# Performance work log

Hardware: AMD Instinct MI355X
Metric: run time of the kernel (lower is better)

Reference implementation:

```python
import jax, jax.numpy as jnp
import numpy as np

VOCAB, EMB, HID, OUT = 100000, 300, 512, 1
B, SEQ = 1, 512


def setup_inputs() -> dict:
    key = jax.random.key(0)
    ks = jax.random.split(key, 8)
    s = 1.0 / np.sqrt(HID)  # torch LSTMCell/Linear init scale
    return {
        "x": jax.random.randint(ks[0], (B, SEQ), 0, VOCAB),
        "h0": jnp.zeros((B, HID), jnp.float32),
        "c0": jnp.zeros((B, HID), jnp.float32),
        "emb_table": jax.random.normal(ks[1], (VOCAB, EMB), jnp.float32) * 0.1,
        "W_ih": jax.random.uniform(ks[2], (4 * HID, EMB), jnp.float32, -s, s),
        "W_hh": jax.random.uniform(ks[3], (4 * HID, HID), jnp.float32, -s, s),
        "b_ih": jax.random.uniform(ks[4], (4 * HID,), jnp.float32, -s, s),
        "b_hh": jax.random.uniform(ks[5], (4 * HID,), jnp.float32, -s, s),
        "fc_w": jax.random.uniform(ks[6], (OUT, HID), jnp.float32, -s, s),
        "fc_b": jax.random.uniform(ks[7], (OUT,), jnp.float32, -s, s),
    }


def reference(x, h0, c0, emb_table, W_ih, W_hh, b_ih, b_hh, fc_w, fc_b):
    embeds = emb_table[x]                      # [B, SEQ, EMB]
    # Faithful to torch: embeds[0][i].view(B, EMB) for i in range(EMB); B == 1.
    steps = embeds[0, :EMB].reshape(EMB, B, EMB)  # [EMB steps, B, EMB]

    def cell(carry, xt):
        h, c = carry
        gates = xt @ W_ih.T + b_ih + h @ W_hh.T + b_hh   # [B, 4*HID]
        i, f, g, o = jnp.split(gates, 4, axis=-1)        # torch gate order i,f,g,o
        i = jax.nn.sigmoid(i)
        f = jax.nn.sigmoid(f)
        g = jnp.tanh(g)
        o = jax.nn.sigmoid(o)
        c = f * c + i * g
        h = o * jnp.tanh(c)
        return (h, c), None

    (h, c), _ = jax.lax.scan(cell, (h0, c0), steps)
    # dropout is identity in eval mode
    out = jax.nn.sigmoid(h @ fc_w.T + fc_b)   # [B, OUT]
    out = out.reshape(B, -1)[:, -1]           # [B]
    return (out, h, c)
```

## Files before the change

### kernel.cpp

```cpp
#include <hip/hip_runtime.h>

#define EMBD 300
#define NSTEP 300
#define HID 512
#define G4 2048
#define NWG 32
#define TPB 256

#define TS2 15
#define NSG 20
#define NRG 8

#define SENTINEL 0xFFC00000u

#define XP_SZ   (NSTEP * G4)
#define HSEQ_OFF XP_SZ

__device__ __forceinline__ float fsig(float x) { return 1.0f / (1.0f + __expf(-x)); }
__device__ __forceinline__ float ftanh(float x) {
    x = fminf(15.0f, fmaxf(-15.0f, x));
    float t = __expf(2.0f * x);
    return (t - 1.0f) / (t + 1.0f);
}

__global__ __launch_bounds__(TPB) void xproj_init_kernel(
    const int* __restrict__ x, const float* __restrict__ h0,
    const float* __restrict__ emb, const float* __restrict__ W_ih,
    const float* __restrict__ b_ih, const float* __restrict__ b_hh,
    float* __restrict__ ws) {
    const int rowg = blockIdx.x;
    const int sg   = blockIdx.y;
    const int tid  = threadIdx.x;
    const int t0   = sg * TS2;
    const int r    = rowg * TPB + tid;

    float* hseq = ws + HSEQ_OFF;

    if (rowg == 0) {
        unsigned* hs = (unsigned*)(hseq + (size_t)(t0 + 1) * HID);
        for (int i = tid; i < TS2 * HID; i += TPB) hs[i] = SENTINEL;
        if (sg == 0) {
            for (int i = tid; i < HID; i += TPB) hseq[i] = h0[i];
        }
    }

    __shared__ float e_lds[TS2][EMBD];
    for (int tt = 0; tt < TS2; ++tt) {
        const float* er = emb + (long long)x[t0 + tt] * EMBD;
        for (int i = tid; i < EMBD; i += TPB) e_lds[tt][i] = er[i];
    }
    __syncthreads();

    float acc[TS2];
    const float bsum = b_ih[r] + b_hh[r];
    #pragma unroll
    for (int tt = 0; tt < TS2; ++tt) acc[tt] = bsum;

    const float* wrow = W_ih + (size_t)r * EMBD;
    for (int e = 0; e < EMBD; e += 4) {
        const float4 w4 = *(const float4*)(wrow + e);
        #pragma unroll
        for (int tt = 0; tt < TS2; ++tt) {
            acc[tt] = fmaf(w4.x, e_lds[tt][e],     acc[tt]);
            acc[tt] = fmaf(w4.y, e_lds[tt][e + 1], acc[tt]);
            acc[tt] = fmaf(w4.z, e_lds[tt][e + 2], acc[tt]);
            acc[tt] = fmaf(w4.w, e_lds[tt][e + 3], acc[tt]);
        }
    }
    #pragma unroll
    for (int tt = 0; tt < TS2; ++tt)
        ws[(size_t)(t0 + tt) * G4 + r] = acc[tt];
}

__global__ __launch_bounds__(TPB, 1) void lstm_scan_kernel(
    const float* __restrict__ c0, const float* __restrict__ W_hh,
    const float* __restrict__ fc_w, const float* __restrict__ fc_b,
    float* __restrict__ ws, float* __restrict__ out) {
    const int tid  = threadIdx.x;
    const int wg   = blockIdx.x;
    const int v    = tid >> 6;
    const int lane = tid & 63;
    const int g    = lane >> 4;
    const int li   = lane & 15;
    const int hidx = wg * 16 + v * 4 + g;

    float* hseq    = ws + HSEQ_OFF;
    const float* xp = ws;

    __shared__ __align__(16) float h_lds[576];

    float wreg[4][32];
    #pragma unroll
    for (int gate = 0; gate < 4; ++gate) {
        const float* wr = W_hh + ((size_t)gate * HID + hidx) * HID + li * 32;
        #pragma unroll
        for (int k = 0; k < 32; k += 4) {
            const float4 w4 = *(const float4*)(wr + k);
            wreg[gate][k] = w4.x; wreg[gate][k + 1] = w4.y;
            wreg[gate][k + 2] = w4.z; wreg[gate][k + 3] = w4.w;
        }
    }

    const bool upd = (li == 0);
    float c = upd ? c0[hidx] : 0.0f;

    for (int s = 0; s < NSTEP; ++s) {
        float xi = 0.f, xf = 0.f, xg = 0.f, xo = 0.f;
        if (upd) {
            const float* xpt = xp + (size_t)s * G4 + hidx;
            xi = xpt[0]; xf = xpt[HID]; xg = xpt[2 * HID]; xo = xpt[3 * HID];
        }

        unsigned* hb = (unsigned*)(hseq + (size_t)s * HID);
        unsigned a = __hip_atomic_load(hb + tid,       __ATOMIC_RELAXED, __HIP_MEMORY_SCOPE_AGENT);
        unsigned b = __hip_atomic_load(hb + tid + 256, __ATOMIC_RELAXED, __HIP_MEMORY_SCOPE_AGENT);
        while (a == SENTINEL || b == SENTINEL) {
            __builtin_amdgcn_s_sleep(1);
            a = __hip_atomic_load(hb + tid,       __ATOMIC_RELAXED, __HIP_MEMORY_SCOPE_AGENT);
            b = __hip_atomic_load(hb + tid + 256, __ATOMIC_RELAXED, __HIP_MEMORY_SCOPE_AGENT);
        }
        const int i0 = tid, i1 = tid + 256;
        h_lds[i0 + ((i0 >> 5) << 2)] = __uint_as_float(a);
        h_lds[i1 + ((i1 >> 5) << 2)] = __uint_as_float(b);
        __syncthreads();

        float sums[4];
        const float* hrow = &h_lds[li * 36];
        #pragma unroll
        for (int gate = 0; gate < 4; ++gate) {
            float acc = 0.0f;
            #pragma unroll
            for (int k = 0; k < 32; k += 4) {
                const float4 h4 = *(const float4*)(hrow + k);
                acc = fmaf(wreg[gate][k],     h4.x, acc);
                acc = fmaf(wreg[gate][k + 1], h4.y, acc);
                acc = fmaf(wreg[gate][k + 2], h4.z, acc);
                acc = fmaf(wreg[gate][k + 3], h4.w, acc);
            }
            acc += __shfl_xor(acc, 1);
            acc += __shfl_xor(acc, 2);
            acc += __shfl_xor(acc, 4);
            acc += __shfl_xor(acc, 8);
            sums[gate] = acc;
        }

        if (upd) {
            const float iv = fsig(sums[0] + xi);
            const float fv = fsig(sums[1] + xf);
            const float gv = ftanh(sums[2] + xg);
            const float ov = fsig(sums[3] + xo);
            c = fv * c + iv * gv;
            const float h = ov * ftanh(c);
            __hip_atomic_store((unsigned*)(hseq + (size_t)(s + 1) * HID + hidx),
                               __float_as_uint(h),
                               __ATOMIC_RELAXED, __HIP_MEMORY_SCOPE_AGENT);
            if (s == NSTEP - 1) {
                out[1 + hidx] = h;
                out[1 + HID + hidx] = c;
            }
        }
        __syncthreads();
    }

    if (wg == 0) {
        __syncthreads();
        unsigned* hf = (unsigned*)(hseq + (size_t)NSTEP * HID);
        unsigned a = __hip_atomic_load(hf + tid,       __ATOMIC_RELAXED, __HIP_MEMORY_SCOPE_AGENT);
        unsigned b = __hip_atomic_load(hf + tid + 256, __ATOMIC_RELAXED, __HIP_MEMORY_SCOPE_AGENT);
        while (a == SENTINEL || b == SENTINEL) {
            __builtin_amdgcn_s_sleep(1);
            a = __hip_atomic_load(hf + tid,       __ATOMIC_RELAXED, __HIP_MEMORY_SCOPE_AGENT);
            b = __hip_atomic_load(hf + tid + 256, __ATOMIC_RELAXED, __HIP_MEMORY_SCOPE_AGENT);
        }
        float p = __uint_as_float(a) * fc_w[tid] + __uint_as_float(b) * fc_w[tid + 256];
        h_lds[tid] = p;
        __syncthreads();
        for (int off = 128; off > 0; off >>= 1) {
            if (tid < off) h_lds[tid] += h_lds[tid + off];
            __syncthreads();
        }
        if (tid == 0) out[0] = fsig(h_lds[0] + fc_b[0]);
    }
}

extern "C" void kernel_launch(void* const* d_in, const int* in_sizes, int n_in,
                              void* d_out, int out_size, void* d_ws, size_t ws_size,
                              hipStream_t stream) {
    (void)in_sizes; (void)n_in; (void)out_size; (void)ws_size;
    const int*   x     = (const int*)d_in[0];
    const float* h0    = (const float*)d_in[1];
    const float* c0    = (const float*)d_in[2];
    const float* emb   = (const float*)d_in[3];
    const float* W_ih  = (const float*)d_in[4];
    const float* W_hh  = (const float*)d_in[5];
    const float* b_ih  = (const float*)d_in[6];
    const float* b_hh  = (const float*)d_in[7];
    const float* fc_w  = (const float*)d_in[8];
    const float* fc_b  = (const float*)d_in[9];
    float* out = (float*)d_out;
    float* ws  = (float*)d_ws;

    xproj_init_kernel<<<dim3(NRG, NSG), dim3(TPB), 0, stream>>>(
        x, h0, emb, W_ih, b_ih, b_hh, ws);
    lstm_scan_kernel<<<dim3(NWG), dim3(TPB), 0, stream>>>(
        c0, W_hh, fc_w, fc_b, ws, out);
}
```

Before: 687.1 us.

## Split LSTM recurrence across 512 threads with double-buffered LDS and packed h exchange

```diff
diff --git a/kernel.cpp b/kernel.cpp
--- a/kernel.cpp
+++ b/kernel.cpp
@@ -4,8 +4,9 @@
 #define NSTEP 300
 #define HID 512
 #define G4 2048
+#define TPB1 256
+#define TPB2 512
 #define NWG 32
-#define TPB 256
 
 #define TS2 15
 #define NSG 20
@@ -13,7 +14,7 @@
 
 #define SENTINEL 0xFFC00000u
 
-#define XP_SZ   (NSTEP * G4)
+#define XP_SZ    (NSTEP * G4)
 #define HSEQ_OFF XP_SZ
 
 __device__ __forceinline__ float fsig(float x) { return 1.0f / (1.0f + __expf(-x)); }
@@ -23,7 +24,7 @@
     return (t - 1.0f) / (t + 1.0f);
 }
 
-__global__ __launch_bounds__(TPB) void xproj_init_kernel(
+__global__ __launch_bounds__(TPB1) void xproj_init_kernel(
     const int* __restrict__ x, const float* __restrict__ h0,
     const float* __restrict__ emb, const float* __restrict__ W_ih,
     const float* __restrict__ b_ih, const float* __restrict__ b_hh,
@@ -32,22 +33,22 @@
     const int sg   = blockIdx.y;
     const int tid  = threadIdx.x;
     const int t0   = sg * TS2;
-    const int r    = rowg * TPB + tid;
+    const int r    = rowg * TPB1 + tid;
 
     float* hseq = ws + HSEQ_OFF;
 
     if (rowg == 0) {
         unsigned* hs = (unsigned*)(hseq + (size_t)(t0 + 1) * HID);
-        for (int i = tid; i < TS2 * HID; i += TPB) hs[i] = SENTINEL;
+        for (int i = tid; i < TS2 * HID; i += TPB1) hs[i] = SENTINEL;
         if (sg == 0) {
-            for (int i = tid; i < HID; i += TPB) hseq[i] = h0[i];
+            for (int i = tid; i < HID; i += TPB1) hseq[i] = h0[i];
         }
     }
 
     __shared__ float e_lds[TS2][EMBD];
     for (int tt = 0; tt < TS2; ++tt) {
         const float* er = emb + (long long)x[t0 + tt] * EMBD;
-        for (int i = tid; i < EMBD; i += TPB) e_lds[tt][i] = er[i];
+        for (int i = tid; i < EMBD; i += TPB1) e_lds[tt][i] = er[i];
     }
     __syncthreads();
 
@@ -72,36 +73,36 @@
         ws[(size_t)(t0 + tt) * G4 + r] = acc[tt];
 }
 
-__global__ __launch_bounds__(TPB, 1) void lstm_scan_kernel(
+__global__ __launch_bounds__(TPB2, 1) void lstm_scan_kernel(
     const float* __restrict__ c0, const float* __restrict__ W_hh,
     const float* __restrict__ fc_w, const float* __restrict__ fc_b,
     float* __restrict__ ws, float* __restrict__ out) {
     const int tid  = threadIdx.x;
     const int wg   = blockIdx.x;
-    const int v    = tid >> 6;
     const int lane = tid & 63;
-    const int g    = lane >> 4;
-    const int li   = lane & 15;
-    const int hidx = wg * 16 + v * 4 + g;
-
-    float* hseq    = ws + HSEQ_OFF;
+    const int grp  = tid >> 5;
+    const int sub  = tid & 31;
+    const int gate = sub >> 3;
+    const int cl   = sub & 7;
+    const int hidx = wg * 16 + grp;
+
+    float* hseq     = ws + HSEQ_OFF;
     const float* xp = ws;
 
-    __shared__ __align__(16) float h_lds[576];
-
-    float wreg[4][32];
-    #pragma unroll
-    for (int gate = 0; gate < 4; ++gate) {
-        const float* wr = W_hh + ((size_t)gate * HID + hidx) * HID + li * 32;
+    __shared__ __align__(16) float h_lds[2][544];
+
+    float wreg[64];
+    {
+        const float* wr = W_hh + ((size_t)gate * HID + hidx) * HID + cl * 64;
         #pragma unroll
-        for (int k = 0; k < 32; k += 4) {
+        for (int k = 0; k < 64; k += 4) {
             const float4 w4 = *(const float4*)(wr + k);
-            wreg[gate][k] = w4.x; wreg[gate][k + 1] = w4.y;
-            wreg[gate][k + 2] = w4.z; wreg[gate][k + 3] = w4.w;
-        }
-    }
-
-    const bool upd = (li == 0);
+            wreg[k] = w4.x; wreg[k + 1] = w4.y;
+            wreg[k + 2] = w4.z; wreg[k + 3] = w4.w;
+        }
+    }
+
+    const bool upd = (sub == 0);
     float c = upd ? c0[hidx] : 0.0f;
 
     for (int s = 0; s < NSTEP; ++s) {
@@ -111,75 +112,89 @@
             xi = xpt[0]; xf = xpt[HID]; xg = xpt[2 * HID]; xo = xpt[3 * HID];
         }
 
-        unsigned* hb = (unsigned*)(hseq + (size_t)s * HID);
-        unsigned a = __hip_atomic_load(hb + tid,       __ATOMIC_RELAXED, __HIP_MEMORY_SCOPE_AGENT);
-        unsigned b = __hip_atomic_load(hb + tid + 256, __ATOMIC_RELAXED, __HIP_MEMORY_SCOPE_AGENT);
-        while (a == SENTINEL || b == SENTINEL) {
-            __builtin_amdgcn_s_sleep(1);
-            a = __hip_atomic_load(hb + tid,       __ATOMIC_RELAXED, __HIP_MEMORY_SCOPE_AGENT);
-            b = __hip_atomic_load(hb + tid + 256, __ATOMIC_RELAXED, __HIP_MEMORY_SCOPE_AGENT);
-        }
-        const int i0 = tid, i1 = tid + 256;
-        h_lds[i0 + ((i0 >> 5) << 2)] = __uint_as_float(a);
-        h_lds[i1 + ((i1 >> 5) << 2)] = __uint_as_float(b);
+        if (tid < 256) {
+            const unsigned long long* slot =
+                (const unsigned long long*)(hseq + (size_t)s * HID) + tid;
+            unsigned long long hv = __hip_atomic_load(slot, __ATOMIC_RELAXED,
+                                                      __HIP_MEMORY_SCOPE_AGENT);
+            while ((unsigned)hv == SENTINEL || (unsigned)(hv >> 32) == SENTINEL) {
+                __builtin_amdgcn_s_sleep(1);
+                hv = __hip_atomic_load(slot, __ATOMIC_RELAXED,
+                                       __HIP_MEMORY_SCOPE_AGENT);
+            }
+            const int i0 = 2 * tid + ((tid >> 5) << 2);
+            *(float2*)&h_lds[s & 1][i0] =
+                make_float2(__uint_as_float((unsigned)hv),
+                            __uint_as_float((unsigned)(hv >> 32)));
+        }
         __syncthreads();
 
-        float sums[4];
-        const float* hrow = &h_lds[li * 36];
+        float acc = 0.0f;
+        const float* hrow = &h_lds[s & 1][cl * 68];
         #pragma unroll
-        for (int gate = 0; gate < 4; ++gate) {
-            float acc = 0.0f;
-            #pragma unroll
-            for (int k = 0; k < 32; k += 4) {
-                const float4 h4 = *(const float4*)(hrow + k);
-                acc = fmaf(wreg[gate][k],     h4.x, acc);
-                acc = fmaf(wreg[gate][k + 1], h4.y, acc);
-                acc = fmaf(wreg[gate][k + 2], h4.z, acc);
-                acc = fmaf(wreg[gate][k + 3], h4.w, acc);
+        for (int k = 0; k < 64; k += 4) {
+            const float4 h4 = *(const float4*)(hrow + k);
+            acc = fmaf(wreg[k],     h4.x, acc);
+            acc = fmaf(wreg[k + 1], h4.y, acc);
+            acc = fmaf(wreg[k + 2], h4.z, acc);
+            acc = fmaf(wreg[k + 3], h4.w, acc);
+        }
+        acc += __shfl_xor(acc, 1);
+        acc += __shfl_xor(acc, 2);
+        acc += __shfl_xor(acc, 4);
+
+        const int base = lane & ~31;
+        const float gi = __shfl(acc, base + 0);
+        const float gf = __shfl(acc, base + 8);
+        const float gg = __shfl(acc, base + 16);
+        const float go = __shfl(acc, base + 24);
+
+        float hnew = 0.0f;
+        if (upd) {
+            const float iv = fsig(gi + xi);
+            const float fv = fsig(gf + xf);
+            const float gv = ftanh(gg + xg);
+            const float ov = fsig(go + xo);
+            c = fv * c + iv * gv;
+            hnew = ov * ftanh(c);
+        }
+        const float hhi = __shfl(hnew, (lane + 32) & 63);
+        if (lane == 0) {
+            const unsigned long long pair =
+                (unsigned long long)__float_as_uint(hnew) |
+                ((unsigned long long)__float_as_uint(hhi) << 32);
+            unsigned long long* dst =
+                (unsigned long long*)(hseq + (size_t)(s + 1) * HID + hidx);
+            __hip_atomic_store(dst, pair, __ATOMIC_RELAXED,
+                               __HIP_MEMORY_SCOPE_AGENT);
+        }
+        if (upd && s == NSTEP - 1) {
+            out[1 + hidx] = hnew;
+            out[1 + HID + hidx] = c;
+        }
+    }
+
+    if (wg == 0) {
+        __shared__ float red[256];
+        if (tid < 256) {
+            const unsigned long long* slot =
+                (const unsigned long long*)(hseq + (size_t)NSTEP * HID) + tid;
+            unsigned long long hv = __hip_atomic_load(slot, __ATOMIC_RELAXED,
+                                                      __HIP_MEMORY_SCOPE_AGENT);
+            while ((unsigned)hv == SENTINEL || (unsigned)(hv >> 32) == SENTINEL) {
+                __builtin_amdgcn_s_sleep(1);
+                hv = __hip_atomic_load(slot, __ATOMIC_RELAXED,
+                                       __HIP_MEMORY_SCOPE_AGENT);
             }
-            acc += __shfl_xor(acc, 1);
-            acc += __shfl_xor(acc, 2);
-            acc += __shfl_xor(acc, 4);
-            acc += __shfl_xor(acc, 8);
-            sums[gate] = acc;
-        }
-
-        if (upd) {
-            const float iv = fsig(sums[0] + xi);
-            const float fv = fsig(sums[1] + xf);
-            const float gv = ftanh(sums[2] + xg);
-            const float ov = fsig(sums[3] + xo);
-            c = fv * c + iv * gv;
-            const float h = ov * ftanh(c);
-            __hip_atomic_store((unsigned*)(hseq + (size_t)(s + 1) * HID + hidx),
-                               __float_as_uint(h),
-                               __ATOMIC_RELAXED, __HIP_MEMORY_SCOPE_AGENT);
-            if (s == NSTEP - 1) {
-                out[1 + hidx] = h;
-                out[1 + HID + hidx] = c;
-            }
-        }
-        __syncthreads();
-    }
-
-    if (wg == 0) {
-        __syncthreads();
-        unsigned* hf = (unsigned*)(hseq + (size_t)NSTEP * HID);
-        unsigned a = __hip_atomic_load(hf + tid,       __ATOMIC_RELAXED, __HIP_MEMORY_SCOPE_AGENT);
-        unsigned b = __hip_atomic_load(hf + tid + 256, __ATOMIC_RELAXED, __HIP_MEMORY_SCOPE_AGENT);
-        while (a == SENTINEL || b == SENTINEL) {
-            __builtin_amdgcn_s_sleep(1);
-            a = __hip_atomic_load(hf + tid,       __ATOMIC_RELAXED, __HIP_MEMORY_SCOPE_AGENT);
-            b = __hip_atomic_load(hf + tid + 256, __ATOMIC_RELAXED, __HIP_MEMORY_SCOPE_AGENT);
-        }
-        float p = __uint_as_float(a) * fc_w[tid] + __uint_as_float(b) * fc_w[tid + 256];
-        h_lds[tid] = p;
+            red[tid] = __uint_as_float((unsigned)hv) * fc_w[2 * tid]
+                     + __uint_as_float((unsigned)(hv >> 32)) * fc_w[2 * tid + 1];
+        }
         __syncthreads();
         for (int off = 128; off > 0; off >>= 1) {
-            if (tid < off) h_lds[tid] += h_lds[tid + off];
+            if (tid < off) red[tid] += red[tid + off];
             __syncthreads();
         }
-        if (tid == 0) out[0] = fsig(h_lds[0] + fc_b[0]);
+        if (tid == 0) out[0] = fsig(red[0] + fc_b[0]);
     }
 }
 
@@ -200,8 +215,8 @@
     float* out = (float*)d_out;
     float* ws  = (float*)d_ws;
 
-    xproj_init_kernel<<<dim3(NRG, NSG), dim3(TPB), 0, stream>>>(
+    xproj_init_kernel<<<dim3(NRG, NSG), dim3(TPB1), 0, stream>>>(
         x, h0, emb, W_ih, b_ih, b_hh, ws);
-    lstm_scan_kernel<<<dim3(NWG), dim3(TPB), 0, stream>>>(
+    lstm_scan_kernel<<<dim3(NWG), dim3(TPB2), 0, stream>>>(
         c0, W_hh, fc_w, fc_b, ws, out);
 }
```

Measured after the change: 820.3 us. 19.4% more time.

## Double-buffer h in LDS, drop trailing barrier, poll with one wave using 64-bit atomics

Applied to the files above, without the earlier changes.

```diff
diff --git a/kernel.cpp b/kernel.cpp
--- a/kernel.cpp
+++ b/kernel.cpp
@@ -4,8 +4,8 @@
 #define NSTEP 300
 #define HID 512
 #define G4 2048
+#define TPB 256
 #define NWG 32
-#define TPB 256
 
 #define TS2 15
 #define NSG 20
@@ -13,7 +13,7 @@
 
 #define SENTINEL 0xFFC00000u
 
-#define XP_SZ   (NSTEP * G4)
+#define XP_SZ    (NSTEP * G4)
 #define HSEQ_OFF XP_SZ
 
 __device__ __forceinline__ float fsig(float x) { return 1.0f / (1.0f + __expf(-x)); }
@@ -84,10 +84,10 @@
     const int li   = lane & 15;
     const int hidx = wg * 16 + v * 4 + g;
 
-    float* hseq    = ws + HSEQ_OFF;
+    float* hseq     = ws + HSEQ_OFF;
     const float* xp = ws;
 
-    __shared__ __align__(16) float h_lds[576];
+    __shared__ __align__(16) float h_lds[2][544];
 
     float wreg[4][32];
     #pragma unroll
@@ -100,6 +100,11 @@
             wreg[gate][k + 2] = w4.z; wreg[gate][k + 3] = w4.w;
         }
     }
+    #pragma unroll
+    for (int gate = 0; gate < 4; ++gate)
+        #pragma unroll
+        for (int k = 0; k < 32; ++k)
+            asm volatile("" : "+v"(wreg[gate][k]));
 
     const bool upd = (li == 0);
     float c = upd ? c0[hidx] : 0.0f;
@@ -111,21 +116,38 @@
             xi = xpt[0]; xf = xpt[HID]; xg = xpt[2 * HID]; xo = xpt[3 * HID];
         }
 
-        unsigned* hb = (unsigned*)(hseq + (size_t)s * HID);
-        unsigned a = __hip_atomic_load(hb + tid,       __ATOMIC_RELAXED, __HIP_MEMORY_SCOPE_AGENT);
-        unsigned b = __hip_atomic_load(hb + tid + 256, __ATOMIC_RELAXED, __HIP_MEMORY_SCOPE_AGENT);
-        while (a == SENTINEL || b == SENTINEL) {
-            __builtin_amdgcn_s_sleep(1);
-            a = __hip_atomic_load(hb + tid,       __ATOMIC_RELAXED, __HIP_MEMORY_SCOPE_AGENT);
-            b = __hip_atomic_load(hb + tid + 256, __ATOMIC_RELAXED, __HIP_MEMORY_SCOPE_AGENT);
-        }
-        const int i0 = tid, i1 = tid + 256;
-        h_lds[i0 + ((i0 >> 5) << 2)] = __uint_as_float(a);
-        h_lds[i1 + ((i1 >> 5) << 2)] = __uint_as_float(b);
+        if (v == 0) {
+            const unsigned long long* slot =
+                (const unsigned long long*)(hseq + (size_t)s * HID) + lane * 4;
+            unsigned long long a0, a1, a2, a3;
+            for (;;) {
+                a0 = __hip_atomic_load(slot + 0, __ATOMIC_RELAXED, __HIP_MEMORY_SCOPE_AGENT);
+                a1 = __hip_atomic_load(slot + 1, __ATOMIC_RELAXED, __HIP_MEMORY_SCOPE_AGENT);
+                a2 = __hip_atomic_load(slot + 2, __ATOMIC_RELAXED, __HIP_MEMORY_SCOPE_AGENT);
+                a3 = __hip_atomic_load(slot + 3, __ATOMIC_RELAXED, __HIP_MEMORY_SCOPE_AGENT);
+                const bool bad =
+                    (unsigned)a0 == SENTINEL || (unsigned)(a0 >> 32) == SENTINEL ||
+                    (unsigned)a1 == SENTINEL || (unsigned)(a1 >> 32) == SENTINEL ||
+                    (unsigned)a2 == SENTINEL || (unsigned)(a2 >> 32) == SENTINEL ||
+                    (unsigned)a3 == SENTINEL || (unsigned)(a3 >> 32) == SENTINEL;
+                if (!bad) break;
+                __builtin_amdgcn_s_sleep(1);
+            }
+            const int base = lane * 8 + ((lane >> 3) << 2);
+            float* dst = &h_lds[s & 1][base];
+            *(float2*)(dst + 0) = make_float2(__uint_as_float((unsigned)a0),
+                                              __uint_as_float((unsigned)(a0 >> 32)));
+            *(float2*)(dst + 2) = make_float2(__uint_as_float((unsigned)a1),
+                                              __uint_as_float((unsigned)(a1 >> 32)));
+            *(float2*)(dst + 4) = make_float2(__uint_as_float((unsigned)a2),
+                                              __uint_as_float((unsigned)(a2 >> 32)));
+            *(float2*)(dst + 6) = make_float2(__uint_as_float((unsigned)a3),
+                                              __uint_as_float((unsigned)(a3 >> 32)));
+        }
         __syncthreads();
 
         float sums[4];
-        const float* hrow = &h_lds[li * 36];
+        const float* hrow = &h_lds[s & 1][li * 32 + ((li >> 1) << 2)];
         #pragma unroll
         for (int gate = 0; gate < 4; ++gate) {
             float acc = 0.0f;
@@ -144,42 +166,49 @@
             sums[gate] = acc;
         }
 
+        float hnew = 0.0f;
         if (upd) {
             const float iv = fsig(sums[0] + xi);
             const float fv = fsig(sums[1] + xf);
             const float gv = ftanh(sums[2] + xg);
             const float ov = fsig(sums[3] + xo);
             c = fv * c + iv * gv;
-            const float h = ov * ftanh(c);
-            __hip_atomic_store((unsigned*)(hseq + (size_t)(s + 1) * HID + hidx),
-                               __float_as_uint(h),
-                               __ATOMIC_RELAXED, __HIP_MEMORY_SCOPE_AGENT);
+            hnew = ov * ftanh(c);
             if (s == NSTEP - 1) {
-                out[1 + hidx] = h;
+                out[1 + hidx] = hnew;
                 out[1 + HID + hidx] = c;
             }
         }
-        __syncthreads();
+        const float hpart = __shfl(hnew, lane + 16);
+        if ((lane & 31) == 0) {
+            const unsigned long long pair =
+                (unsigned long long)__float_as_uint(hnew) |
+                ((unsigned long long)__float_as_uint(hpart) << 32);
+            unsigned long long* dst = (unsigned long long*)
+                (hseq + (size_t)(s + 1) * HID + wg * 16 + v * 4 + (lane >> 4));
+            __hip_atomic_store(dst, pair, __ATOMIC_RELAXED, __HIP_MEMORY_SCOPE_AGENT);
+        }
     }
 
     if (wg == 0) {
-        __syncthreads();
-        unsigned* hf = (unsigned*)(hseq + (size_t)NSTEP * HID);
-        unsigned a = __hip_atomic_load(hf + tid,       __ATOMIC_RELAXED, __HIP_MEMORY_SCOPE_AGENT);
-        unsigned b = __hip_atomic_load(hf + tid + 256, __ATOMIC_RELAXED, __HIP_MEMORY_SCOPE_AGENT);
-        while (a == SENTINEL || b == SENTINEL) {
+        __shared__ float red[256];
+        const unsigned long long* slot =
+            (const unsigned long long*)(hseq + (size_t)NSTEP * HID) + tid;
+        unsigned long long hv = __hip_atomic_load(slot, __ATOMIC_RELAXED,
+                                                  __HIP_MEMORY_SCOPE_AGENT);
+        while ((unsigned)hv == SENTINEL || (unsigned)(hv >> 32) == SENTINEL) {
             __builtin_amdgcn_s_sleep(1);
-            a = __hip_atomic_load(hf + tid,       __ATOMIC_RELAXED, __HIP_MEMORY_SCOPE_AGENT);
-            b = __hip_atomic_load(hf + tid + 256, __ATOMIC_RELAXED, __HIP_MEMORY_SCOPE_AGENT);
-        }
-        float p = __uint_as_float(a) * fc_w[tid] + __uint_as_float(b) * fc_w[tid + 256];
-        h_lds[tid] = p;
+            hv = __hip_atomic_load(slot, __ATOMIC_RELAXED,
+                                   __HIP_MEMORY_SCOPE_AGENT);
+        }
+        red[tid] = __uint_as_float((unsigned)hv) * fc_w[2 * tid]
+                 + __uint_as_float((unsigned)(hv >> 32)) * fc_w[2 * tid + 1];
         __syncthreads();
         for (int off = 128; off > 0; off >>= 1) {
-            if (tid < off) h_lds[tid] += h_lds[tid + off];
+            if (tid < off) red[tid] += red[tid + off];
             __syncthreads();
         }
-        if (tid == 0) out[0] = fsig(h_lds[0] + fc_b[0]);
+        if (tid == 0) out[0] = fsig(red[0] + fc_b[0]);
     }
 }
 
```

After: 699.2 us. Within noise of the previous version (+1.8%).
